# Kernel optimization log

Hardware: AMD Instinct MI355X
Metric: run time of the kernel (lower is better)

## Reference

```python
import jax, jax.numpy as jnp
import numpy as np

D_MODEL = 1024
D_STATE = 16
D_CONV = 4
EXPAND = 2
D_INNER = EXPAND * D_MODEL          # 2048
DT_RANK = (D_MODEL + 15) // 16      # 64
B_SZ, SEQ = 2, 1024
LN_EPS = 1e-6


def setup_inputs() -> dict:
    key = jax.random.key(0)
    ks = jax.random.split(key, 12)
    s = 0.02
    x = jax.random.normal(ks[0], (B_SZ, SEQ, D_MODEL), dtype=jnp.float32)
    W_in = jax.random.normal(ks[1], (D_MODEL, 2 * D_INNER), dtype=jnp.float32) * s
    conv_w = jax.random.normal(ks[2], (D_INNER, D_CONV), dtype=jnp.float32) * s
    conv_b = jnp.zeros((D_INNER,), dtype=jnp.float32)
    W_xproj = jax.random.normal(ks[3], (D_INNER, DT_RANK + 2 * D_STATE), dtype=jnp.float32) * s
    W_dt = jax.random.normal(ks[4], (DT_RANK, D_INNER), dtype=jnp.float32) * (DT_RANK ** -0.5)
    # dt bias ~ log-uniform init as in Mamba (softplus^-1 of dt in [1e-3, 1e-1])
    dt = jnp.exp(jax.random.uniform(ks[5], (D_INNER,)) * (np.log(0.1) - np.log(1e-3)) + np.log(1e-3))
    b_dt = dt + jnp.log(-jnp.expm1(-dt))  # inverse softplus
    A_log = jnp.log(jnp.broadcast_to(jnp.arange(1, D_STATE + 1, dtype=jnp.float32), (D_INNER, D_STATE)))
    D_param = jnp.ones((D_INNER,), dtype=jnp.float32)
    W_out = jax.random.normal(ks[6], (D_INNER, D_MODEL), dtype=jnp.float32) * s
    gamma = jnp.ones((D_MODEL,), dtype=jnp.float32)
    beta = jnp.zeros((D_MODEL,), dtype=jnp.float32)
    return {"x": x, "W_in": W_in, "conv_w": conv_w, "conv_b": conv_b,
            "W_xproj": W_xproj, "W_dt": W_dt, "b_dt": b_dt, "A_log": A_log,
            "D_param": D_param, "W_out": W_out, "gamma": gamma, "beta": beta}


def _mamba(x, W_in, conv_w, conv_b, W_xproj, W_dt, b_dt, A_log, D_param, W_out):
    B, L, _ = x.shape
    xz = x @ W_in                                  # [B,L,2*d_inner]
    xi, z = jnp.split(xz, 2, axis=-1)              # [B,L,d_inner] each
    # causal depthwise conv1d, kernel D_CONV
    xp = jnp.pad(xi, ((0, 0), (D_CONV - 1, 0), (0, 0)))
    xc = conv_b
    for k in range(D_CONV):
        xc = xc + xp[:, k:k + L, :] * conv_w[:, k]
    xc = jax.nn.silu(xc)                           # [B,L,d_inner]
    x_dbl = xc @ W_xproj                           # [B,L,dt_rank+2*d_state]
    dt_r = x_dbl[..., :DT_RANK]
    B_ssm = x_dbl[..., DT_RANK:DT_RANK + D_STATE]  # [B,L,d_state]
    C_ssm = x_dbl[..., DT_RANK + D_STATE:]         # [B,L,d_state]
    dt = jax.nn.softplus(dt_r @ W_dt + b_dt)       # [B,L,d_inner]
    A = -jnp.exp(A_log)                            # [d_inner,d_state]
    dA = jnp.exp(dt[..., None] * A)                # [B,L,d_inner,d_state]
    dBu = dt[..., None] * B_ssm[:, :, None, :] * xc[..., None]
    # selective scan over time (time-major for lax.scan)
    dA_t = jnp.moveaxis(dA, 1, 0)                  # [L,B,d_inner,d_state]
    dBu_t = jnp.moveaxis(dBu, 1, 0)
    C_t = jnp.moveaxis(C_ssm, 1, 0)                # [L,B,d_state]
    h0 = jnp.zeros((B, D_INNER, D_STATE), dtype=x.dtype)

    def step(h, inp):
        a, bu, c = inp
        h = a * h + bu
        y = jnp.einsum('bdn,bn->bd', h, c)
        return h, y

    _, ys = jax.lax.scan(step, h0, (dA_t, dBu_t, C_t))
    y = jnp.moveaxis(ys, 0, 1)                     # [B,L,d_inner]
    y = y + xc * D_param
    y = y * jax.nn.silu(z)
    return y @ W_out                               # [B,L,d_model]


def reference(x, W_in, conv_w, conv_b, W_xproj, W_dt, b_dt, A_log, D_param, W_out, gamma, beta):
    m = _mamba(x, W_in, conv_w, conv_b, W_xproj, W_dt, b_dt, A_log, D_param, W_out)
    mu = jnp.mean(m, axis=-1, keepdims=True)
    var = jnp.mean(jnp.square(m - mu), axis=-1, keepdims=True)
    ln = (m - mu) * jax.lax.rsqrt(var + LN_EPS) * gamma + beta
    return x + ln
```

## Files before the change

kernel.cpp:

```cpp
#include <hip/hip_runtime.h>
#include <math.h>

#define DM   1024
#define DI   2048
#define DS   16
#define DTR  64
#define NB   2
#define SEQL 1024
#define NTOK (NB*SEQL)
#define XND  96
#define XNP  128
#define CK   128
#define CL   8

typedef __bf16 bf16x8 __attribute__((ext_vector_type(8)));
typedef __bf16 bf16x4 __attribute__((ext_vector_type(4)));
typedef float  f32x4  __attribute__((ext_vector_type(4)));

#define PREP_BLOCKS 3872

__device__ inline void trans_tile64(const float* __restrict__ W,
                                    __bf16* __restrict__ WT, int K, int N,
                                    int n0, int k0, int tid, __bf16 (*t)[65])
{
    const int tx = tid & 63, ty = tid >> 6;
    #pragma unroll
    for (int i = 0; i < 16; i++)
        t[ty * 16 + i][tx] = (__bf16)W[(size_t)(k0 + ty * 16 + i) * N + n0 + tx];
    __syncthreads();
    #pragma unroll
    for (int i = 0; i < 16; i++)
        WT[(size_t)(n0 + ty * 16 + i) * K + k0 + tx] = t[tx][ty * 16 + i];
}

__global__ __launch_bounds__(256) void prep(
    const float* __restrict__ x, const float* __restrict__ W_in,
    const float* __restrict__ W_out, const float* __restrict__ W_dt,
    const float* __restrict__ W_xprj,
    __bf16* __restrict__ xb, __bf16* __restrict__ W_inT,
    __bf16* __restrict__ W_outT, __bf16* __restrict__ WdtT,
    __bf16* __restrict__ W_xprT, float* __restrict__ xdbl)
{
    __shared__ __bf16 t[64][65];
    int bid = blockIdx.x;
    const int tid = threadIdx.x;

    if (bid < 256) {
        const int i = bid * 1024 + tid * 4;
        const float4 z = {0.f, 0.f, 0.f, 0.f};
        *reinterpret_cast<float4*>(&xdbl[i]) = z;
        return;
    }
    bid -= 256;
    if (bid < 1024) {
        const int e = (bid * 256 + tid) * 8;
        const float4 v0 = *reinterpret_cast<const float4*>(&x[e]);
        const float4 v1 = *reinterpret_cast<const float4*>(&x[e + 4]);
        bf16x8 o;
        o[0] = (__bf16)v0.x; o[1] = (__bf16)v0.y; o[2] = (__bf16)v0.z; o[3] = (__bf16)v0.w;
        o[4] = (__bf16)v1.x; o[5] = (__bf16)v1.y; o[6] = (__bf16)v1.z; o[7] = (__bf16)v1.w;
        *reinterpret_cast<bf16x8*>(&xb[e]) = o;
        return;
    }
    bid -= 1024;
    if (bid < 1024) {
        trans_tile64(W_in, W_inT, DM, 2 * DI, (bid & 63) * 64, (bid >> 6) * 64, tid, t);
        return;
    }
    bid -= 1024;
    if (bid < 512) {
        trans_tile64(W_out, W_outT, DI, DM, (bid & 15) * 64, (bid >> 4) * 64, tid, t);
        return;
    }
    bid -= 512;
    if (bid < 32) {
        trans_tile64(W_dt, WdtT, DTR, DI, bid * 64, 0, tid, t);
        return;
    }
    bid -= 32;
    {
        const int idx = bid * 256 + tid;
        const int k = idx & (DI - 1);
        const int n = idx >> 11;
        W_xprT[(size_t)n * DI + k] = (n < XND) ? (__bf16)W_xprj[(size_t)k * XND + n]
                                               : (__bf16)0.f;
    }
}

template<int MODE, int SWZ>
__global__ __launch_bounds__(256) void gemm_bf16(
    const __bf16* __restrict__ A, const __bf16* __restrict__ Bt,
    void* __restrict__ Cp, int M, int N, int K, int ldc,
    const float* __restrict__ bias)
{
    __shared__ __bf16 As[2][128 * 64];
    __shared__ __bf16 Bs[2][128 * 64];
    const int tid  = threadIdx.x;
    const int lane = tid & 63;
    const int wid  = tid >> 6;
    const int wr   = wid >> 1, wc = wid & 1;

    int bx = blockIdx.x, by = blockIdx.y;
    if (SWZ != 0) {
        const int gx = gridDim.x, gy = gridDim.y;
        const int nxy = gx * gy;
        const int q = nxy >> 3;
        int lin = by * gx + bx;
        lin = (lin & 7) * q + (lin >> 3);
        if (SWZ == 1) { by = lin / gx; bx = lin % gx; }
        else          { bx = lin / gy; by = lin % gy; }
    }
    const int brow = by * 128, bcol = bx * 128;
    const int kper = K / gridDim.z;
    const int kbeg = blockIdx.z * kper, kend = kbeg + kper;

    f32x4 acc[4][4] = {};

    auto stage = [&](int buf, int k0) {
        if (MODE == 2) {
            const float* Af = reinterpret_cast<const float*>(A);
            #pragma unroll
            for (int p = 0; p < 4; p++) {
                const int i = p * 256 + tid;
                const int r = i >> 3;
                const int j = i & 7;
                const float4 v0 = *reinterpret_cast<const float4*>(
                    &Af[(size_t)(brow + r) * XNP + j * 8]);
                const float4 v1 = *reinterpret_cast<const float4*>(
                    &Af[(size_t)(brow + r) * XNP + j * 8 + 4]);
                bf16x8 o;
                o[0] = (__bf16)v0.x; o[1] = (__bf16)v0.y; o[2] = (__bf16)v0.z; o[3] = (__bf16)v0.w;
                o[4] = (__bf16)v1.x; o[5] = (__bf16)v1.y; o[6] = (__bf16)v1.z; o[7] = (__bf16)v1.w;
                *reinterpret_cast<bf16x8*>(&As[buf][r * 64 + ((j ^ (r & 7))) * 8]) = o;
            }
        } else {
            #pragma unroll
            for (int p = 0; p < 4; p++) {
                const int i = p * 256 + tid;
                const int r = i >> 3;
                const int gc = ((i & 7) ^ (r & 7)) * 8;
                __builtin_amdgcn_global_load_lds(
                    (const __attribute__((address_space(1))) void*)(A + (size_t)(brow + r) * K + k0 + gc),
                    (__attribute__((address_space(3))) void*)(&As[buf][i * 8]), 16, 0, 0);
            }
        }
        #pragma unroll
        for (int p = 0; p < 4; p++) {
            const int i = p * 256 + tid;
            const int r = i >> 3;
            const int gc = ((i & 7) ^ (r & 7)) * 8;
            __builtin_amdgcn_global_load_lds(
                (const __attribute__((address_space(1))) void*)(Bt + (size_t)(bcol + r) * K + k0 + gc),
                (__attribute__((address_space(3))) void*)(&Bs[buf][i * 8]), 16, 0, 0);
        }
    };

    const int nt = (kend - kbeg) >> 6;
    stage(0, kbeg);
    __syncthreads();
    int cur = 0;
    for (int t = 0; t < nt; t++) {
        if (t + 1 < nt) stage(cur ^ 1, kbeg + ((t + 1) << 6));
        const __bf16* Ab = &As[cur][0];
        const __bf16* Bb = &Bs[cur][0];
        bf16x8 a[2][4], b[2][4];
        const int rA = wr * 64 + (lane & 15);
        const int rB = wc * 64 + (lane & 15);
        const int cq = lane >> 4;
        const int rx = lane & 7;
        #pragma unroll
        for (int ks = 0; ks < 2; ks++) {
            const int sl = ((ks * 4 + cq) ^ rx) * 8;
            #pragma unroll
            for (int m = 0; m < 4; m++) {
                a[ks][m] = *reinterpret_cast<const bf16x8*>(&Ab[(rA + m * 16) * 64 + sl]);
                b[ks][m] = *reinterpret_cast<const bf16x8*>(&Bb[(rB + m * 16) * 64 + sl]);
            }
        }
        #pragma unroll
        for (int ks = 0; ks < 2; ks++)
            #pragma unroll
            for (int m = 0; m < 4; m++)
                #pragma unroll
                for (int n = 0; n < 4; n++)
                    acc[m][n] = __builtin_amdgcn_mfma_f32_16x16x32_bf16(
                        a[ks][m], b[ks][n], acc[m][n], 0, 0, 0);
        __syncthreads();
        cur ^= 1;
    }
    const int crow = brow + wr * 64 + (lane >> 4) * 4;
    const int ccol = bcol + wc * 64 + (lane & 15);
    __bf16* Cb3 = (__bf16*)Cp + (size_t)blockIdx.z * ((MODE == 3) ? (size_t)M * ldc : 0);
    #pragma unroll
    for (int m = 0; m < 4; m++)
        #pragma unroll
        for (int n = 0; n < 4; n++) {
            const int col = ccol + n * 16;
            #pragma unroll
            for (int j = 0; j < 4; j++) {
                const size_t idx = (size_t)(crow + m * 16 + j) * ldc + col;
                if (MODE == 0) {
                    ((float*)Cp)[idx] = acc[m][n][j];
                } else if (MODE == 1) {
                    atomicAdd(&((float*)Cp)[idx], acc[m][n][j]);
                } else if (MODE == 2) {
                    const float v = acc[m][n][j] + bias[col];
                    ((__bf16*)Cp)[idx] =
                        (__bf16)(fmaxf(v, 0.f) + log1pf(__expf(-fabsf(v))));
                } else {
                    Cb3[idx] = (__bf16)acc[m][n][j];
                }
            }
        }
}

__global__ __launch_bounds__(256) void conv_silu(
    const __bf16* __restrict__ xzb, const float* __restrict__ conv_w,
    const float* __restrict__ conv_b, __bf16* __restrict__ xcb)
{
    const int g  = blockIdx.x * 256 + threadIdx.x;
    const int d0 = (g & 255) * 8;
    const int tok = g >> 8;
    const int t   = tok & (SEQL - 1);

    float4 wv[8];
    #pragma unroll
    for (int j = 0; j < 8; j++)
        wv[j] = *reinterpret_cast<const float4*>(&conv_w[(d0 + j) * 4]);
    float acc[8];
    {
        const float4 b0 = *reinterpret_cast<const float4*>(&conv_b[d0]);
        const float4 b1 = *reinterpret_cast<const float4*>(&conv_b[d0 + 4]);
        acc[0] = b0.x; acc[1] = b0.y; acc[2] = b0.z; acc[3] = b0.w;
        acc[4] = b1.x; acc[5] = b1.y; acc[6] = b1.z; acc[7] = b1.w;
    }
    #pragma unroll
    for (int k = 0; k < 4; k++) {
        const int tt = t + k - 3;
        if (tt >= 0) {
            const bf16x8 v = *reinterpret_cast<const bf16x8*>(
                &xzb[(size_t)(tok + k - 3) * (2 * DI) + d0]);
            #pragma unroll
            for (int j = 0; j < 8; j++) {
                const float wk = (k == 0) ? wv[j].x : (k == 1) ? wv[j].y
                               : (k == 2) ? wv[j].z : wv[j].w;
                acc[j] += (float)v[j] * wk;
            }
        }
    }
    bf16x8 o;
    #pragma unroll
    for (int j = 0; j < 8; j++) {
        const float a = acc[j];
        o[j] = (__bf16)(a / (1.f + __expf(-a)));
    }
    *reinterpret_cast<bf16x8*>(&xcb[(size_t)g * 8]) = o;
}

__global__ __launch_bounds__(256) void scan_partial(
    const __bf16* __restrict__ xcb, const float* __restrict__ xdbl,
    const __bf16* __restrict__ dtb, const float* __restrict__ A_log,
    __bf16* __restrict__ hpart, float* __restrict__ sdtb)
{
    __shared__ float Bsh[CL][16];
    const int tid = threadIdx.x;
    const int d = blockIdx.x * 256 + tid;
    const int c = blockIdx.y, b = blockIdx.z;
    const size_t base = (size_t)b * SEQL + c * CL;
    {
        const int st = tid >> 4, sg = tid & 15;
        if (st < CL) Bsh[st][sg] = xdbl[(base + st) * XNP + DTR + sg];
    }
    float dtv[CL], xcv[CL];
    #pragma unroll
    for (int t = 0; t < CL; t++) {
        dtv[t] = (float)dtb[(base + t) * DI + d];
        xcv[t] = (float)xcb[(base + t) * DI + d];
    }
    float Av[16];
    #pragma unroll
    for (int i = 0; i < 4; i++) {
        const float4 v = *reinterpret_cast<const float4*>(&A_log[(size_t)d * 16 + i * 4]);
        Av[i*4+0] = -__expf(v.x); Av[i*4+1] = -__expf(v.y);
        Av[i*4+2] = -__expf(v.z); Av[i*4+3] = -__expf(v.w);
    }
    __syncthreads();
    float h[16] = {};
    float sdt = 0.f;
    #pragma unroll
    for (int t = 0; t < CL; t++) {
        sdt += dtv[t];
        const float dx = dtv[t] * xcv[t];
        #pragma unroll
        for (int n = 0; n < 16; n++)
            h[n] = __expf(dtv[t] * Av[n]) * h[n] + dx * Bsh[t][n];
    }
    const size_t ob = ((size_t)(b * CK + c) * DI + d) * 16;
    bf16x8 o0, o1;
    #pragma unroll
    for (int i = 0; i < 8; i++) { o0[i] = (__bf16)h[i]; o1[i] = (__bf16)h[i + 8]; }
    *reinterpret_cast<bf16x8*>(&hpart[ob])     = o0;
    *reinterpret_cast<bf16x8*>(&hpart[ob + 8]) = o1;
    sdtb[(size_t)(b * CK + c) * DI + d] = sdt;
}

__global__ __launch_bounds__(256) void scan_combine(
    const float* __restrict__ A_log, const float* __restrict__ sdtb,
    const __bf16* __restrict__ hpart, __bf16* __restrict__ hentry)
{
    const int idx = blockIdx.x * 256 + threadIdx.x;
    const int n = idx & 15;
    const int d = (idx >> 4) & (DI - 1);
    const int b = idx >> 15;
    const float A = -__expf(A_log[(size_t)d * 16 + n]);
    float h = 0.f;
    for (int cb = 0; cb < CK / 16; cb++) {
        float hl[16], sv[16];
        #pragma unroll
        for (int j = 0; j < 16; j++) {
            const int c = cb * 16 + j;
            hl[j] = (float)hpart[((size_t)(b * CK + c) * DI + d) * 16 + n];
            sv[j] = sdtb[(size_t)(b * CK + c) * DI + d];
        }
        #pragma unroll
        for (int j = 0; j < 16; j++) {
            const int c = cb * 16 + j;
            hentry[((size_t)(b * CK + c) * DI + d) * 16 + n] = (__bf16)h;
            h = __expf(A * sv[j]) * h + hl[j];
        }
    }
}

__global__ __launch_bounds__(256) void scan_final(
    const __bf16* __restrict__ xzb, const __bf16* __restrict__ xcb,
    const float* __restrict__ xdbl, const __bf16* __restrict__ dtb,
    const float* __restrict__ A_log, const float* __restrict__ Dp,
    const __bf16* __restrict__ hentry, __bf16* __restrict__ yb)
{
    __shared__ float Bsh[CL][16];
    __shared__ float Csh[CL][16];
    const int tid = threadIdx.x;
    const int d = blockIdx.x * 256 + tid;
    const int c = blockIdx.y, b = blockIdx.z;
    const size_t base = (size_t)b * SEQL + c * CL;
    {
        const int st = tid >> 4, sg = tid & 15;
        if (st < CL)
            Bsh[st][sg] = xdbl[(base + st) * XNP + DTR + sg];
        else if (st < 2 * CL)
            Csh[st - CL][sg] = xdbl[(base + st - CL) * XNP + DTR + DS + sg];
    }
    float dtv[CL], xcv[CL], zv[CL];
    #pragma unroll
    for (int t = 0; t < CL; t++) {
        dtv[t] = (float)dtb[(base + t) * DI + d];
        xcv[t] = (float)xcb[(base + t) * DI + d];
        zv[t]  = (float)xzb[(base + t) * (2 * DI) + DI + d];
    }
    float Av[16];
    #pragma unroll
    for (int i = 0; i < 4; i++) {
        const float4 v = *reinterpret_cast<const float4*>(&A_log[(size_t)d * 16 + i * 4]);
        Av[i*4+0] = -__expf(v.x); Av[i*4+1] = -__expf(v.y);
        Av[i*4+2] = -__expf(v.z); Av[i*4+3] = -__expf(v.w);
    }
    float h[16];
    const size_t ob = ((size_t)(b * CK + c) * DI + d) * 16;
    {
        const bf16x8 v0 = *reinterpret_cast<const bf16x8*>(&hentry[ob]);
        const bf16x8 v1 = *reinterpret_cast<const bf16x8*>(&hentry[ob + 8]);
        #pragma unroll
        for (int i = 0; i < 8; i++) { h[i] = (float)v0[i]; h[i + 8] = (float)v1[i]; }
    }
    const float Dv = Dp[d];
    __syncthreads();
    #pragma unroll
    for (int t = 0; t < CL; t++) {
        const float dx = dtv[t] * xcv[t];
        float y = 0.f;
        #pragma unroll
        for (int n = 0; n < 16; n++) {
            h[n] = __expf(dtv[t] * Av[n]) * h[n] + dx * Bsh[t][n];
            y += h[n] * Csh[t][n];
        }
        y += xcv[t] * Dv;
        y *= zv[t] / (1.f + __expf(-zv[t]));
        yb[(base + t) * DI + d] = (__bf16)y;
    }
}

__global__ __launch_bounds__(256) void ln_add(
    const float* __restrict__ x, const __bf16* __restrict__ mpart,
    const float* __restrict__ gamma, const float* __restrict__ beta,
    float* __restrict__ out)
{
    const int tok = blockIdx.x;
    const int tid = threadIdx.x;
    const int lane = tid & 63, wave = tid >> 6;
    __shared__ float red[4];
    __shared__ float stats[2];

    float4 v = {0.f, 0.f, 0.f, 0.f};
    #pragma unroll
    for (int p = 0; p < 4; p++) {
        const bf16x4 mv = *reinterpret_cast<const bf16x4*>(
            &mpart[((size_t)p * NTOK + tok) * DM + tid * 4]);
        v.x += (float)mv[0]; v.y += (float)mv[1];
        v.z += (float)mv[2]; v.w += (float)mv[3];
    }
    float s = v.x + v.y + v.z + v.w;
    #pragma unroll
    for (int o = 32; o > 0; o >>= 1) s += __shfl_down(s, o, 64);
    if (lane == 0) red[wave] = s;
    __syncthreads();
    if (tid == 0) stats[0] = (red[0] + red[1] + red[2] + red[3]) * (1.f / DM);
    __syncthreads();
    const float mu = stats[0];
    const float dx = v.x - mu, dy = v.y - mu, dz = v.z - mu, dw = v.w - mu;
    float q = dx * dx + dy * dy + dz * dz + dw * dw;
    #pragma unroll
    for (int o = 32; o > 0; o >>= 1) q += __shfl_down(q, o, 64);
    if (lane == 0) red[wave] = q;
    __syncthreads();
    if (tid == 0)
        stats[1] = rsqrtf((red[0] + red[1] + red[2] + red[3]) * (1.f / DM) + 1e-6f);
    __syncthreads();
    const float rs = stats[1];

    const float4 g  = reinterpret_cast<const float4*>(gamma)[tid];
    const float4 bb = reinterpret_cast<const float4*>(beta)[tid];
    const float4 xv = reinterpret_cast<const float4*>(&x[(size_t)tok * DM])[tid];
    float4 o;
    o.x = xv.x + dx * rs * g.x + bb.x;
    o.y = xv.y + dy * rs * g.y + bb.y;
    o.z = xv.z + dz * rs * g.z + bb.z;
    o.w = xv.w + dw * rs * g.w + bb.w;
    reinterpret_cast<float4*>(&out[(size_t)tok * DM])[tid] = o;
}

extern "C" void kernel_launch(void* const* d_in, const int* in_sizes, int n_in,
                              void* d_out, int out_size, void* d_ws, size_t ws_size,
                              hipStream_t stream)
{
    const float* x      = (const float*)d_in[0];
    const float* W_in   = (const float*)d_in[1];
    const float* conv_w = (const float*)d_in[2];
    const float* conv_b = (const float*)d_in[3];
    const float* W_xprj = (const float*)d_in[4];
    const float* W_dt   = (const float*)d_in[5];
    const float* b_dt   = (const float*)d_in[6];
    const float* A_log  = (const float*)d_in[7];
    const float* D_par  = (const float*)d_in[8];
    const float* W_out  = (const float*)d_in[9];
    const float* gamma  = (const float*)d_in[10];
    const float* beta   = (const float*)d_in[11];
    float* out = (float*)d_out;

    char* w = (char*)d_ws;
    __bf16* xzb    = (__bf16*)(w + 0);
    __bf16* xcb    = (__bf16*)(w + 16777216);
    float*  xdbl   = (float*) (w + 25165824);
    __bf16* dtb    = (__bf16*)(w + 26214400);
    __bf16* mpart  = (__bf16*)(w + 34603008);
    __bf16* hpart  = (__bf16*)(w + 51380224);
    __bf16* hentry = (__bf16*)(w + 68157440);
    float*  sdtb   = (float*) (w + 84934656);
    __bf16* xb     = (__bf16*)(w + 87031808);
    __bf16* W_inT  = (__bf16*)(w + 91226112);
    __bf16* W_outT = (__bf16*)(w + 99614720);
    __bf16* W_xprT = (__bf16*)(w + 103809024);
    __bf16* WdtT   = (__bf16*)(w + 104333312);
    __bf16* yb     = (__bf16*)(w + 104595456);

    prep<<<PREP_BLOCKS, 256, 0, stream>>>(
        x, W_in, W_out, W_dt, W_xprj, xb, W_inT, W_outT, WdtT, W_xprT, xdbl);

    gemm_bf16<3, 2><<<dim3(32, 16, 1), 256, 0, stream>>>(
        xb, W_inT, xzb, NTOK, 2 * DI, DM, 2 * DI, nullptr);

    conv_silu<<<(NTOK * DI / 8) / 256, 256, 0, stream>>>(xzb, conv_w, conv_b, xcb);

    gemm_bf16<1, 0><<<dim3(1, 16, 16), 256, 0, stream>>>(
        xcb, W_xprT, xdbl, NTOK, XNP, DI, XNP, nullptr);

    gemm_bf16<2, 0><<<dim3(16, 16, 1), 256, 0, stream>>>(
        (const __bf16*)xdbl, WdtT, dtb, NTOK, DI, DTR, DI, b_dt);

    scan_partial<<<dim3(DI / 256, CK, NB), 256, 0, stream>>>(
        xcb, xdbl, dtb, A_log, hpart, sdtb);
    scan_combine<<<NB * DI * DS / 256, 256, 0, stream>>>(A_log, sdtb, hpart, hentry);
    scan_final<<<dim3(DI / 256, CK, NB), 256, 0, stream>>>(
        xzb, xcb, xdbl, dtb, A_log, D_par, hentry, yb);

    gemm_bf16<3, 1><<<dim3(8, 16, 4), 256, 0, stream>>>(
        yb, W_outT, mpart, NTOK, DM, DI, DM, nullptr);

    ln_add<<<NTOK, 256, 0, stream>>>(x, mpart, gamma, beta, out);
}
```

Baseline: 162.1 us.

## Parameterize GEMM N-tile width and drop LDS double buffering

Makes the GEMM's N tile width a template parameter and launches the in-projection, dt-projection and out-projection GEMMs with 64-wide tiles on grids twice as large, so more blocks are resident across the CUs. It also removes the double-buffered LDS staging and uses a single buffer with a sync before and after each load, which cuts shared memory per block and may raise occupancy. In exchange, global-to-LDS loads no longer overlap with MFMA compute, and each A tile is reused across fewer output columns, so A traffic grows.

```diff
diff --git a/kernel.cpp b/kernel.cpp
--- a/kernel.cpp
+++ b/kernel.cpp
@@ -87,14 +87,15 @@
     }
 }
 
-template<int MODE, int SWZ>
+template<int MODE, int SWZ, int TN>
 __global__ __launch_bounds__(256) void gemm_bf16(
     const __bf16* __restrict__ A, const __bf16* __restrict__ Bt,
     void* __restrict__ Cp, int M, int N, int K, int ldc,
     const float* __restrict__ bias)
 {
-    __shared__ __bf16 As[2][128 * 64];
-    __shared__ __bf16 Bs[2][128 * 64];
+    constexpr int NFR = TN / 32;
+    __shared__ __bf16 As[128 * 64];
+    __shared__ __bf16 Bs[TN * 64];
     const int tid  = threadIdx.x;
     const int lane = tid & 63;
     const int wid  = tid >> 6;
@@ -110,13 +111,14 @@
         if (SWZ == 1) { by = lin / gx; bx = lin % gx; }
         else          { bx = lin / gy; by = lin % gy; }
     }
-    const int brow = by * 128, bcol = bx * 128;
+    const int brow = by * 128, bcol = bx * TN;
     const int kper = K / gridDim.z;
     const int kbeg = blockIdx.z * kper, kend = kbeg + kper;
 
-    f32x4 acc[4][4] = {};
-
-    auto stage = [&](int buf, int k0) {
+    f32x4 acc[4][NFR] = {};
+
+    for (int k0 = kbeg; k0 < kend; k0 += 64) {
+        __syncthreads();
         if (MODE == 2) {
             const float* Af = reinterpret_cast<const float*>(A);
             #pragma unroll
@@ -131,7 +133,7 @@
                 bf16x8 o;
                 o[0] = (__bf16)v0.x; o[1] = (__bf16)v0.y; o[2] = (__bf16)v0.z; o[3] = (__bf16)v0.w;
                 o[4] = (__bf16)v1.x; o[5] = (__bf16)v1.y; o[6] = (__bf16)v1.z; o[7] = (__bf16)v1.w;
-                *reinterpret_cast<bf16x8*>(&As[buf][r * 64 + ((j ^ (r & 7))) * 8]) = o;
+                *reinterpret_cast<bf16x8*>(&As[r * 64 + ((j ^ (r & 7))) * 8]) = o;
             }
         } else {
             #pragma unroll
@@ -141,60 +143,50 @@
                 const int gc = ((i & 7) ^ (r & 7)) * 8;
                 __builtin_amdgcn_global_load_lds(
                     (const __attribute__((address_space(1))) void*)(A + (size_t)(brow + r) * K + k0 + gc),
-                    (__attribute__((address_space(3))) void*)(&As[buf][i * 8]), 16, 0, 0);
+                    (__attribute__((address_space(3))) void*)(&As[i * 8]), 16, 0, 0);
             }
         }
         #pragma unroll
-        for (int p = 0; p < 4; p++) {
+        for (int p = 0; p < TN / 32; p++) {
             const int i = p * 256 + tid;
             const int r = i >> 3;
             const int gc = ((i & 7) ^ (r & 7)) * 8;
             __builtin_amdgcn_global_load_lds(
                 (const __attribute__((address_space(1))) void*)(Bt + (size_t)(bcol + r) * K + k0 + gc),
-                (__attribute__((address_space(3))) void*)(&Bs[buf][i * 8]), 16, 0, 0);
-        }
-    };
-
-    const int nt = (kend - kbeg) >> 6;
-    stage(0, kbeg);
-    __syncthreads();
-    int cur = 0;
-    for (int t = 0; t < nt; t++) {
-        if (t + 1 < nt) stage(cur ^ 1, kbeg + ((t + 1) << 6));
-        const __bf16* Ab = &As[cur][0];
-        const __bf16* Bb = &Bs[cur][0];
-        bf16x8 a[2][4], b[2][4];
+                (__attribute__((address_space(3))) void*)(&Bs[i * 8]), 16, 0, 0);
+        }
+        __syncthreads();
+        bf16x8 a[2][4], b[2][NFR];
         const int rA = wr * 64 + (lane & 15);
-        const int rB = wc * 64 + (lane & 15);
+        const int rB = wc * (TN / 2) + (lane & 15);
         const int cq = lane >> 4;
         const int rx = lane & 7;
         #pragma unroll
         for (int ks = 0; ks < 2; ks++) {
             const int sl = ((ks * 4 + cq) ^ rx) * 8;
             #pragma unroll
-            for (int m = 0; m < 4; m++) {
-                a[ks][m] = *reinterpret_cast<const bf16x8*>(&Ab[(rA + m * 16) * 64 + sl]);
-                b[ks][m] = *reinterpret_cast<const bf16x8*>(&Bb[(rB + m * 16) * 64 + sl]);
-            }
+            for (int m = 0; m < 4; m++)
+                a[ks][m] = *reinterpret_cast<const bf16x8*>(&As[(rA + m * 16) * 64 + sl]);
+            #pragma unroll
+            for (int n = 0; n < NFR; n++)
+                b[ks][n] = *reinterpret_cast<const bf16x8*>(&Bs[(rB + n * 16) * 64 + sl]);
         }
         #pragma unroll
         for (int ks = 0; ks < 2; ks++)
             #pragma unroll
             for (int m = 0; m < 4; m++)
                 #pragma unroll
-                for (int n = 0; n < 4; n++)
+                for (int n = 0; n < NFR; n++)
                     acc[m][n] = __builtin_amdgcn_mfma_f32_16x16x32_bf16(
                         a[ks][m], b[ks][n], acc[m][n], 0, 0, 0);
-        __syncthreads();
-        cur ^= 1;
     }
     const int crow = brow + wr * 64 + (lane >> 4) * 4;
-    const int ccol = bcol + wc * 64 + (lane & 15);
+    const int ccol = bcol + wc * (TN / 2) + (lane & 15);
     __bf16* Cb3 = (__bf16*)Cp + (size_t)blockIdx.z * ((MODE == 3) ? (size_t)M * ldc : 0);
     #pragma unroll
     for (int m = 0; m < 4; m++)
         #pragma unroll
-        for (int n = 0; n < 4; n++) {
+        for (int n = 0; n < NFR; n++) {
             const int col = ccol + n * 16;
             #pragma unroll
             for (int j = 0; j < 4; j++) {
@@ -475,15 +467,15 @@
     prep<<<PREP_BLOCKS, 256, 0, stream>>>(
         x, W_in, W_out, W_dt, W_xprj, xb, W_inT, W_outT, WdtT, W_xprT, xdbl);
 
-    gemm_bf16<3, 2><<<dim3(32, 16, 1), 256, 0, stream>>>(
+    gemm_bf16<3, 2, 64><<<dim3(64, 16, 1), 256, 0, stream>>>(
         xb, W_inT, xzb, NTOK, 2 * DI, DM, 2 * DI, nullptr);
 
     conv_silu<<<(NTOK * DI / 8) / 256, 256, 0, stream>>>(xzb, conv_w, conv_b, xcb);
 
-    gemm_bf16<1, 0><<<dim3(1, 16, 16), 256, 0, stream>>>(
+    gemm_bf16<1, 0, 128><<<dim3(1, 16, 16), 256, 0, stream>>>(
         xcb, W_xprT, xdbl, NTOK, XNP, DI, XNP, nullptr);
 
-    gemm_bf16<2, 0><<<dim3(16, 16, 1), 256, 0, stream>>>(
+    gemm_bf16<2, 0, 64><<<dim3(32, 16, 1), 256, 0, stream>>>(
         (const __bf16*)xdbl, WdtT, dtb, NTOK, DI, DTR, DI, b_dt);
 
     scan_partial<<<dim3(DI / 256, CK, NB), 256, 0, stream>>>(
@@ -492,7 +484,7 @@
     scan_final<<<dim3(DI / 256, CK, NB), 256, 0, stream>>>(
         xzb, xcb, xdbl, dtb, A_log, D_par, hentry, yb);
 
-    gemm_bf16<3, 1><<<dim3(8, 16, 4), 256, 0, stream>>>(
+    gemm_bf16<3, 1, 64><<<dim3(16, 16, 4), 256, 0, stream>>>(
         yb, W_outT, mpart, NTOK, DM, DI, DM, nullptr);
 
     ln_add<<<NTOK, 256, 0, stream>>>(x, mpart, gamma, beta, out);
```

Result: no change. 162.8 us (+0.4%).
